# Kernel tuning notes

Measured on AMD Instinct MI355X. Metric: run time of the kernel, lower is better.

Reference implementation:

```python
import jax, jax.numpy as jnp
import numpy as np

B, HEADS, HEAD_DIM, WS = 64, 6, 32, 8
POS_DIM = 12  # (dim//4)//4 = 192//16
N = WS ** 3


def _ln(x, g, b, eps=1e-5):
    mu = jnp.mean(x, axis=-1, keepdims=True)
    var = jnp.var(x, axis=-1, keepdims=True)
    return (x - mu) / jnp.sqrt(var + eps) * g + b


def setup_inputs() -> dict:
    key = jax.random.key(0)
    ks = jax.random.split(key, 10)
    s = 0.02
    inp = {
        'q': jax.random.normal(ks[0], (B, HEADS, N, HEAD_DIM), jnp.float32),
        'k': jax.random.normal(ks[1], (B, HEADS, N, HEAD_DIM), jnp.float32),
        'v': jax.random.normal(ks[2], (B, HEADS, N, HEAD_DIM), jnp.float32),
        'h': WS, 'w': WS, 'd': WS,
        'pos_proj_w': jax.random.normal(ks[3], (3, POS_DIM), jnp.float32) * s,
        'pos_proj_b': jnp.zeros((POS_DIM,), jnp.float32),
        'ln1_g': jnp.ones((POS_DIM,), jnp.float32),
        'ln1_b': jnp.zeros((POS_DIM,), jnp.float32),
        'w1': jax.random.normal(ks[4], (POS_DIM, POS_DIM), jnp.float32) * s,
        'b1': jnp.zeros((POS_DIM,), jnp.float32),
        'ln2_g': jnp.ones((POS_DIM,), jnp.float32),
        'ln2_b': jnp.zeros((POS_DIM,), jnp.float32),
        'w2': jax.random.normal(ks[5], (POS_DIM, POS_DIM), jnp.float32) * s,
        'b2': jnp.zeros((POS_DIM,), jnp.float32),
        'ln3_g': jnp.ones((POS_DIM,), jnp.float32),
        'ln3_b': jnp.zeros((POS_DIM,), jnp.float32),
        'w3': jax.random.normal(ks[6], (POS_DIM, HEADS), jnp.float32) * s,
        'b3': jnp.zeros((HEADS,), jnp.float32),
    }
    return inp


def reference(q, k, v, h, w, d,
              pos_proj_w, pos_proj_b,
              ln1_g, ln1_b, w1, b1,
              ln2_g, ln2_b, w2, b2,
              ln3_g, ln3_b, w3, b3):
    scale = HEAD_DIM ** (-0.5)
    attn = jnp.einsum('bhnc,bhmc->bhnm', q * scale, k)

    # candidate relative offsets table: ((2h-1)(2w-1)(2d-1), 3)
    bh = jnp.arange(1 - h, h, dtype=jnp.float32)
    bw = jnp.arange(1 - w, w, dtype=jnp.float32)
    bd = jnp.arange(1 - d, d, dtype=jnp.float32)
    biases = jnp.stack(jnp.meshgrid(bh, bw, bd, indexing='ij')).reshape(3, -1).T

    # per-pair relative index (faithfully sums the 3 shifted coords, as source does)
    coords = jnp.stack(jnp.meshgrid(jnp.arange(h), jnp.arange(w), jnp.arange(d),
                                    indexing='ij')).reshape(3, -1)  # (3, N)
    rel = coords[:, :, None] - coords[:, None, :]  # (3, N, N)
    rel_idx = (rel[0] + h - 1) + (rel[1] + w - 1) + (rel[2] + d - 1)  # (N, N)

    # dynamic pos-bias MLP
    x = biases @ pos_proj_w + pos_proj_b
    x = jax.nn.relu(_ln(x, ln1_g, ln1_b)) @ w1 + b1
    x = jax.nn.relu(_ln(x, ln2_g, ln2_b)) @ w2 + b2
    pos = jax.nn.relu(_ln(x, ln3_g, ln3_b)) @ w3 + b3  # (table, heads)

    rpb = pos[rel_idx]                       # (N, N, heads) gather
    attn = attn + jnp.transpose(rpb, (2, 0, 1))[None]  # (1, heads, N, N)

    attn = jax.nn.softmax(attn, axis=-1)
    return jnp.einsum('bhnm,bhmc->bhnc', attn, v)
```

## Files before the change

kernel.cpp:

```cpp
#include <hip/hip_runtime.h>
#include <math.h>

typedef _Float16 h8 __attribute__((ext_vector_type(8)));
typedef _Float16 h4 __attribute__((ext_vector_type(4)));
typedef float    f4 __attribute__((ext_vector_type(4)));

#define NHEADS 6
#define HDIM   32
#define NTOK   512
#define NTAB   43
#define LOG2E  1.44269504088896340736f

__device__ inline int ds3(int x) {
  return (x >> 6) + ((x >> 3) & 7) + (x & 7);
}

__device__ inline void ln_relu12(const float* x, float* t, const float* g, const float* b) {
  float mu = 0.f;
#pragma unroll
  for (int j = 0; j < 12; j++) mu += x[j];
  mu *= (1.f / 12.f);
  float var = 0.f;
#pragma unroll
  for (int j = 0; j < 12; j++) { float d = x[j] - mu; var += d * d; }
  var *= (1.f / 12.f);
  float inv = rsqrtf(var + 1e-5f);
#pragma unroll
  for (int j = 0; j < 12; j++) {
    float y = (x[j] - mu) * inv * g[j] + b[j];
    t[j] = y > 0.f ? y : 0.f;
  }
}

__device__ inline void mm12(const float* t, float* x, const float* w, const float* c) {
#pragma unroll
  for (int j = 0; j < 12; j++) {
    float acc = c[j];
#pragma unroll
    for (int i = 0; i < 12; i++) acc += t[i] * w[i * 12 + j];
    x[j] = acc;
  }
}

__global__ __launch_bounds__(256)
void fused_attn_kernel(const float* __restrict__ q, const float* __restrict__ k,
                       const float* __restrict__ v,
                       const float* __restrict__ pw, const float* __restrict__ pb,
                       const float* __restrict__ g1, const float* __restrict__ b1,
                       const float* __restrict__ w1, const float* __restrict__ c1,
                       const float* __restrict__ g2, const float* __restrict__ b2,
                       const float* __restrict__ w2, const float* __restrict__ c2,
                       const float* __restrict__ g3, const float* __restrict__ b3,
                       const float* __restrict__ w3, const float* __restrict__ c3,
                       float* __restrict__ out)
{
  __shared__ __align__(16) char smem[4][2][2304];
  __shared__ f4 posw4r[NTAB];
  __shared__ float posb_s[NTAB * NHEADS];
  __shared__ __align__(16) _Float16 Ks[2][64 * 40];
  __shared__ __align__(16) _Float16 Vt[2][32 * 72];

  const int tid  = threadIdx.x;
  const int wave = tid >> 6;
  const int lane = tid & 63;
  const int quad = lane >> 4;
  const int l16  = lane & 15;
  const int bh   = blockIdx.x;
  const int h    = bh % NHEADS;
  const int qq   = blockIdx.y;
  const float SC = 0.17677669529663687f * LOG2E;

  const long bhbase = (long)bh * NTOK * HDIM;
  const float4* kg = (const float4*)(k + bhbase);
  const float4* vg = (const float4*)(v + bhbase);

  if (tid < NTAB) {
    const float bh_ = -7.0f;
    const float bw_ = (float)(tid / 15) - 7.0f;
    const float bd_ = (float)(tid % 15) - 7.0f;
    float x[12], t[12];
#pragma unroll
    for (int j = 0; j < 12; j++)
      x[j] = bh_ * pw[j] + bw_ * pw[12 + j] + bd_ * pw[24 + j] + pb[j];
    ln_relu12(x, t, g1, b1); mm12(t, x, w1, c1);
    ln_relu12(x, t, g2, b2); mm12(t, x, w2, c2);
    ln_relu12(x, t, g3, b3);
#pragma unroll
    for (int hd = 0; hd < NHEADS; hd++) {
      float acc = c3[hd];
#pragma unroll
      for (int i = 0; i < 12; i++) acc += t[i] * w3[i * NHEADS + hd];
      posb_s[tid * NHEADS + hd] = acc * LOG2E;
    }
  }

#pragma unroll
  for (int i = 0; i < 2; i++) {
    int f = i * 256 + tid, row = f >> 3, c4 = f & 7;
    float4 e = kg[f];
    h4 eh = { (_Float16)e.x, (_Float16)e.y, (_Float16)e.z, (_Float16)e.w };
    *(h4*)&Ks[0][row * 40 + c4 * 4] = eh;
    float4 w = vg[f];
    Vt[0][(c4 * 4 + 0) * 72 + row] = (_Float16)w.x;
    Vt[0][(c4 * 4 + 1) * 72 + row] = (_Float16)w.y;
    Vt[0][(c4 * 4 + 2) * 72 + row] = (_Float16)w.z;
    Vt[0][(c4 * 4 + 3) * 72 + row] = (_Float16)w.w;
  }
  __syncthreads();

  if (tid >= 3 && tid < NTAB) {
    f4 pv = { posb_s[tid * NHEADS + h],       posb_s[(tid - 1) * NHEADS + h],
              posb_s[(tid - 2) * NHEADS + h], posb_s[(tid - 3) * NHEADS + h] };
    posw4r[tid] = pv;
  }

  int qt[2] = { qq * 8 + wave * 2, qq * 8 + wave * 2 + 1 };
  h8 qf[2];
  int qs21[2];
#pragma unroll
  for (int ti = 0; ti < 2; ti++) {
    const float* qrow = q + bhbase + (long)(qt[ti] * 16 + l16) * HDIM + quad * 8;
    float4 a = *(const float4*)qrow;
    float4 b = *(const float4*)(qrow + 4);
    h8 qh = { (_Float16)(a.x * SC), (_Float16)(a.y * SC),
              (_Float16)(a.z * SC), (_Float16)(a.w * SC),
              (_Float16)(b.x * SC), (_Float16)(b.y * SC),
              (_Float16)(b.z * SC), (_Float16)(b.w * SC) };
    qf[ti] = qh;
    qs21[ti] = ds3(qt[ti] * 16) + (l16 >> 3) + (l16 & 7) + 21;
  }
  const int kdq = (quad >> 1) + (quad & 1) * 4;

  f4 o[2][2];
#pragma unroll
  for (int ti = 0; ti < 2; ti++) { o[ti][0] = f4{0,0,0,0}; o[ti][1] = f4{0,0,0,0}; }
  float lp[2] = {0.f, 0.f};

  __syncthreads();

#pragma unroll 2
  for (int kc = 0; kc < 8; kc++) {
    const int cur = kc & 1;

    float4 kreg0, kreg1, vreg0, vreg1;
    if (kc < 7) {
      const int fb = (kc + 1) * 512 + tid;
      kreg0 = kg[fb];       kreg1 = kg[fb + 256];
      vreg0 = vg[fb];       vreg1 = vg[fb + 256];
    }

    h8 kf[4];
    h4 vA[2][4];
#pragma unroll
    for (int t = 0; t < 4; t++)
      kf[t] = *(const h8*)&Ks[cur][(t * 16 + l16) * 40 + quad * 8];
#pragma unroll
    for (int hf = 0; hf < 2; hf++)
#pragma unroll
      for (int t = 0; t < 4; t++)
        vA[hf][t] = *(const h4*)&Vt[cur][(hf * 16 + l16) * 72 + t * 16 + quad * 4];

#pragma unroll
    for (int ti = 0; ti < 2; ti++) {
      f4 s[4];
#pragma unroll
      for (int t = 0; t < 4; t++) {
        int idx0 = qs21[ti] - (kc + t * 2 + kdq);
        f4 cin = posw4r[idx0];
        s[t] = __builtin_amdgcn_mfma_f32_16x16x32_f16(kf[t], qf[ti], cin, 0, 0, 0);
      }
      h4 pk[4];
#pragma unroll
      for (int t = 0; t < 4; t++) {
        float p0 = __builtin_amdgcn_exp2f(s[t][0]);
        float p1 = __builtin_amdgcn_exp2f(s[t][1]);
        float p2 = __builtin_amdgcn_exp2f(s[t][2]);
        float p3 = __builtin_amdgcn_exp2f(s[t][3]);
        lp[ti] += (p0 + p1) + (p2 + p3);
        pk[t] = h4{ (_Float16)p0, (_Float16)p1, (_Float16)p2, (_Float16)p3 };
      }
#pragma unroll
      for (int t = 0; t < 4; t++) {
        o[ti][0] = __builtin_amdgcn_mfma_f32_16x16x16f16(vA[0][t], pk[t], o[ti][0], 0, 0, 0);
        o[ti][1] = __builtin_amdgcn_mfma_f32_16x16x16f16(vA[1][t], pk[t], o[ti][1], 0, 0, 0);
      }
    }

    if (kc < 7) {
      const int nb = cur ^ 1;
#pragma unroll
      for (int i = 0; i < 2; i++) {
        float4 e = (i == 0) ? kreg0 : kreg1;
        float4 w = (i == 0) ? vreg0 : vreg1;
        int f = i * 256 + tid, row = f >> 3, c4 = f & 7;
        h4 eh = { (_Float16)e.x, (_Float16)e.y, (_Float16)e.z, (_Float16)e.w };
        *(h4*)&Ks[nb][row * 40 + c4 * 4] = eh;
        Vt[nb][(c4 * 4 + 0) * 72 + row] = (_Float16)w.x;
        Vt[nb][(c4 * 4 + 1) * 72 + row] = (_Float16)w.y;
        Vt[nb][(c4 * 4 + 2) * 72 + row] = (_Float16)w.z;
        Vt[nb][(c4 * 4 + 3) * 72 + row] = (_Float16)w.w;
      }
      __syncthreads();
    }
  }

#pragma unroll
  for (int ti = 0; ti < 2; ti++) {
    float l = lp[ti];
    l += __shfl_xor(l, 16);
    l += __shfl_xor(l, 32);
    const float inv = 1.f / l;
    float* os = (float*)smem[wave][ti];
    f4 w0 = { o[ti][0][0] * inv, o[ti][0][1] * inv, o[ti][0][2] * inv, o[ti][0][3] * inv };
    f4 w1 = { o[ti][1][0] * inv, o[ti][1][1] * inv, o[ti][1][2] * inv, o[ti][1][3] * inv };
    *(f4*)&os[l16 * 36 + quad * 4]      = w0;
    *(f4*)&os[l16 * 36 + 16 + quad * 4] = w1;
    const int q_ = lane >> 2, seg = lane & 3;
    f4 r0 = *(const f4*)&os[q_ * 36 + seg * 8];
    f4 r1 = *(const f4*)&os[q_ * 36 + seg * 8 + 4];
    float* orow = out + (long)bh * NTOK * HDIM + (long)(qt[ti] * 16 + q_) * HDIM + seg * 8;
    *(float4*)orow       = *(float4*)&r0;
    *(float4*)(orow + 4) = *(float4*)&r1;
  }
}

extern "C" void kernel_launch(void* const* d_in, const int* in_sizes, int n_in,
                              void* d_out, int out_size, void* d_ws, size_t ws_size,
                              hipStream_t stream) {
  (void)in_sizes; (void)n_in; (void)out_size; (void)d_ws; (void)ws_size;
  const float* q  = (const float*)d_in[0];
  const float* k  = (const float*)d_in[1];
  const float* v  = (const float*)d_in[2];
  const float* pw  = (const float*)d_in[6];
  const float* pb  = (const float*)d_in[7];
  const float* g1  = (const float*)d_in[8];
  const float* b1  = (const float*)d_in[9];
  const float* w1  = (const float*)d_in[10];
  const float* c1  = (const float*)d_in[11];
  const float* g2  = (const float*)d_in[12];
  const float* b2  = (const float*)d_in[13];
  const float* w2  = (const float*)d_in[14];
  const float* c2  = (const float*)d_in[15];
  const float* g3  = (const float*)d_in[16];
  const float* b3  = (const float*)d_in[17];
  const float* w3  = (const float*)d_in[18];
  const float* c3  = (const float*)d_in[19];
  float* outp = (float*)d_out;

  fused_attn_kernel<<<dim3(384, 4), 256, 0, stream>>>(
      q, k, v,
      pw, pb, g1, b1, w1, c1, g2, b2, w2, c2, g3, b3, w3, c3, outp);
}
```

Before: 172.1 us.

## Stage full V in LDS upfront, read K directly from global, drop per-chunk syncs

The whole transposed V for the head is now loaded into a single 32x516 LDS buffer before the main loop, replacing the double-buffered per-chunk K/V staging. K fragments are read from global memory straight into registers each iteration, which removes the K LDS tiles and all per-chunk barriers. The output is written directly from the MFMA accumulators instead of going through an LDS transpose. The cost is a longer serialized prologue with no overlap between V loads and compute, uncoalesced global K reads (each block re-reading K from cache), less coalesced output stores, and higher LDS use that may reduce occupancy.

```diff
diff --git a/kernel.cpp b/kernel.cpp
--- a/kernel.cpp
+++ b/kernel.cpp
@@ -10,6 +10,7 @@
 #define NTOK   512
 #define NTAB   43
 #define LOG2E  1.44269504088896340736f
+#define VP     516
 
 __device__ inline int ds3(int x) {
   return (x >> 6) + ((x >> 3) & 7) + (x & 7);
@@ -54,24 +55,21 @@
                        const float* __restrict__ w3, const float* __restrict__ c3,
                        float* __restrict__ out)
 {
-  __shared__ __align__(16) char smem[4][2][2304];
+  __shared__ __align__(16) _Float16 Vt[32 * VP];
   __shared__ f4 posw4r[NTAB];
   __shared__ float posb_s[NTAB * NHEADS];
-  __shared__ __align__(16) _Float16 Ks[2][64 * 40];
-  __shared__ __align__(16) _Float16 Vt[2][32 * 72];
 
   const int tid  = threadIdx.x;
-  const int wave = tid >> 6;
   const int lane = tid & 63;
   const int quad = lane >> 4;
   const int l16  = lane & 15;
   const int bh   = blockIdx.x;
   const int h    = bh % NHEADS;
   const int qq   = blockIdx.y;
+  const int wave = tid >> 6;
   const float SC = 0.17677669529663687f * LOG2E;
 
   const long bhbase = (long)bh * NTOK * HDIM;
-  const float4* kg = (const float4*)(k + bhbase);
   const float4* vg = (const float4*)(v + bhbase);
 
   if (tid < NTAB) {
@@ -94,24 +92,14 @@
     }
   }
 
-#pragma unroll
-  for (int i = 0; i < 2; i++) {
+#pragma unroll 4
+  for (int i = 0; i < 16; i++) {
     int f = i * 256 + tid, row = f >> 3, c4 = f & 7;
-    float4 e = kg[f];
-    h4 eh = { (_Float16)e.x, (_Float16)e.y, (_Float16)e.z, (_Float16)e.w };
-    *(h4*)&Ks[0][row * 40 + c4 * 4] = eh;
     float4 w = vg[f];
-    Vt[0][(c4 * 4 + 0) * 72 + row] = (_Float16)w.x;
-    Vt[0][(c4 * 4 + 1) * 72 + row] = (_Float16)w.y;
-    Vt[0][(c4 * 4 + 2) * 72 + row] = (_Float16)w.z;
-    Vt[0][(c4 * 4 + 3) * 72 + row] = (_Float16)w.w;
-  }
-  __syncthreads();
-
-  if (tid >= 3 && tid < NTAB) {
-    f4 pv = { posb_s[tid * NHEADS + h],       posb_s[(tid - 1) * NHEADS + h],
-              posb_s[(tid - 2) * NHEADS + h], posb_s[(tid - 3) * NHEADS + h] };
-    posw4r[tid] = pv;
+    Vt[(c4 * 4 + 0) * VP + row] = (_Float16)w.x;
+    Vt[(c4 * 4 + 1) * VP + row] = (_Float16)w.y;
+    Vt[(c4 * 4 + 2) * VP + row] = (_Float16)w.z;
+    Vt[(c4 * 4 + 3) * VP + row] = (_Float16)w.w;
   }
 
   int qt[2] = { qq * 8 + wave * 2, qq * 8 + wave * 2 + 1 };
@@ -131,6 +119,14 @@
   }
   const int kdq = (quad >> 1) + (quad & 1) * 4;
 
+  __syncthreads();
+
+  if (tid >= 3 && tid < NTAB) {
+    f4 pv = { posb_s[tid * NHEADS + h],       posb_s[(tid - 1) * NHEADS + h],
+              posb_s[(tid - 2) * NHEADS + h], posb_s[(tid - 3) * NHEADS + h] };
+    posw4r[tid] = pv;
+  }
+
   f4 o[2][2];
 #pragma unroll
   for (int ti = 0; ti < 2; ti++) { o[ti][0] = f4{0,0,0,0}; o[ti][1] = f4{0,0,0,0}; }
@@ -140,25 +136,21 @@
 
 #pragma unroll 2
   for (int kc = 0; kc < 8; kc++) {
-    const int cur = kc & 1;
-
-    float4 kreg0, kreg1, vreg0, vreg1;
-    if (kc < 7) {
-      const int fb = (kc + 1) * 512 + tid;
-      kreg0 = kg[fb];       kreg1 = kg[fb + 256];
-      vreg0 = vg[fb];       vreg1 = vg[fb + 256];
-    }
-
     h8 kf[4];
+#pragma unroll
+    for (int t = 0; t < 4; t++) {
+      const float* krow = k + bhbase + (long)(kc * 64 + t * 16 + l16) * HDIM + quad * 8;
+      float4 a = *(const float4*)krow;
+      float4 b = *(const float4*)(krow + 4);
+      kf[t] = h8{ (_Float16)a.x, (_Float16)a.y, (_Float16)a.z, (_Float16)a.w,
+                  (_Float16)b.x, (_Float16)b.y, (_Float16)b.z, (_Float16)b.w };
+    }
     h4 vA[2][4];
 #pragma unroll
-    for (int t = 0; t < 4; t++)
-      kf[t] = *(const h8*)&Ks[cur][(t * 16 + l16) * 40 + quad * 8];
-#pragma unroll
     for (int hf = 0; hf < 2; hf++)
 #pragma unroll
       for (int t = 0; t < 4; t++)
-        vA[hf][t] = *(const h4*)&Vt[cur][(hf * 16 + l16) * 72 + t * 16 + quad * 4];
+        vA[hf][t] = *(const h4*)&Vt[(hf * 16 + l16) * VP + kc * 64 + t * 16 + quad * 4];
 
 #pragma unroll
     for (int ti = 0; ti < 2; ti++) {
@@ -185,23 +177,6 @@
         o[ti][1] = __builtin_amdgcn_mfma_f32_16x16x16f16(vA[1][t], pk[t], o[ti][1], 0, 0, 0);
       }
     }
-
-    if (kc < 7) {
-      const int nb = cur ^ 1;
-#pragma unroll
-      for (int i = 0; i < 2; i++) {
-        float4 e = (i == 0) ? kreg0 : kreg1;
-        float4 w = (i == 0) ? vreg0 : vreg1;
-        int f = i * 256 + tid, row = f >> 3, c4 = f & 7;
-        h4 eh = { (_Float16)e.x, (_Float16)e.y, (_Float16)e.z, (_Float16)e.w };
-        *(h4*)&Ks[nb][row * 40 + c4 * 4] = eh;
-        Vt[nb][(c4 * 4 + 0) * 72 + row] = (_Float16)w.x;
-        Vt[nb][(c4 * 4 + 1) * 72 + row] = (_Float16)w.y;
-        Vt[nb][(c4 * 4 + 2) * 72 + row] = (_Float16)w.z;
-        Vt[nb][(c4 * 4 + 3) * 72 + row] = (_Float16)w.w;
-      }
-      __syncthreads();
-    }
   }
 
 #pragma unroll
@@ -210,17 +185,13 @@
     l += __shfl_xor(l, 16);
     l += __shfl_xor(l, 32);
     const float inv = 1.f / l;
-    float* os = (float*)smem[wave][ti];
-    f4 w0 = { o[ti][0][0] * inv, o[ti][0][1] * inv, o[ti][0][2] * inv, o[ti][0][3] * inv };
-    f4 w1 = { o[ti][1][0] * inv, o[ti][1][1] * inv, o[ti][1][2] * inv, o[ti][1][3] * inv };
-    *(f4*)&os[l16 * 36 + quad * 4]      = w0;
-    *(f4*)&os[l16 * 36 + 16 + quad * 4] = w1;
-    const int q_ = lane >> 2, seg = lane & 3;
-    f4 r0 = *(const f4*)&os[q_ * 36 + seg * 8];
-    f4 r1 = *(const f4*)&os[q_ * 36 + seg * 8 + 4];
-    float* orow = out + (long)bh * NTOK * HDIM + (long)(qt[ti] * 16 + q_) * HDIM + seg * 8;
-    *(float4*)orow       = *(float4*)&r0;
-    *(float4*)(orow + 4) = *(float4*)&r1;
+#pragma unroll
+    for (int hf = 0; hf < 2; hf++) {
+      f4 w = { o[ti][hf][0] * inv, o[ti][hf][1] * inv,
+               o[ti][hf][2] * inv, o[ti][hf][3] * inv };
+      float* orow = out + bhbase + (long)(qt[ti] * 16 + l16) * HDIM + hf * 16 + quad * 4;
+      *(float4*)orow = *(float4*)&w;
+    }
   }
 }
 
```

Result: slower. 187.0 us (+8.6%).
